# Kernel tuning notes

Hardware: AMD Instinct MI355X
Metric: run time of the kernel (lower is better)

Reference implementation:

```python
import jax, jax.numpy as jnp
import numpy as np

EMBED = 768
HEADS = 8


def setup_inputs() -> dict:
    key = jax.random.key(0)
    k1, k2, k3 = jax.random.split(key, 3)
    x = jax.random.normal(k1, (16, 1024, EMBED), dtype=jnp.float32)
    W_qkv = jax.random.normal(k2, (EMBED, 3 * EMBED), dtype=jnp.float32) * 0.02
    b_qkv = jnp.zeros((3 * EMBED,), dtype=jnp.float32)
    W_fc = jax.random.normal(k3, (EMBED, EMBED), dtype=jnp.float32) * 0.02
    b_fc = jnp.zeros((EMBED,), dtype=jnp.float32)
    return {"x": x, "W_qkv": W_qkv, "b_qkv": b_qkv, "W_fc": W_fc, "b_fc": b_fc}


def reference(x, W_qkv, b_qkv, W_fc, b_fc):
    b, n, e = x.shape
    h = HEADS
    d = e // h
    # fused QKV projection: (b, n, 3e) -> (b, n, h, d, 3) -> (3, b, h, n, d)
    qkv = x @ W_qkv + b_qkv
    qkv = qkv.reshape(b, n, h, d, 3)
    q, k, v = jnp.transpose(qkv, (4, 0, 2, 1, 3))
    # raw attention scores (b, h, n, n)
    qkt = jnp.einsum('bhid,bhjd->bhij', q, k)
    # NOTE: the original module computes softmax(QKT)/sqrt(E) into `attention`
    # but then uses the RAW scores QKT for the value contraction. We replicate
    # that faithfully; the softmax is dead code w.r.t. the output (p=0 dropout).
    attention = jax.nn.softmax(qkt, axis=-1) / jnp.sqrt(jnp.float32(e))  # unused, DCE'd
    z = jnp.einsum('bhik,bhkd->bhid', qkt, v)  # (b, h, n, d)
    z = jnp.transpose(z, (0, 2, 1, 3)).reshape(b, n, e)
    out = z @ W_fc + b_fc
    return out
```

## Files before the change

kernel.cpp:

```cpp
#include <hip/hip_runtime.h>

typedef unsigned short u16;
typedef __attribute__((ext_vector_type(8))) __bf16 bf16x8;
typedef __attribute__((ext_vector_type(4))) float f32x4;

__device__ __forceinline__ u16 f2bf(float f) {
  union { float f; unsigned u; } x; x.f = f;
  unsigned r = x.u + 0x7fffu + ((x.u >> 16) & 1u);
  return (u16)(r >> 16);
}

#define GLD16(g, l) __builtin_amdgcn_global_load_lds( \
    (__attribute__((address_space(1))) void*)(size_t)(g), \
    (__attribute__((address_space(3))) void*)(l), 16, 0, 0)

__global__ __launch_bounds__(256) void prep(const float* __restrict__ x,
                                            u16* __restrict__ xz,
                                            const float* __restrict__ Wqkv,
                                            u16* __restrict__ wqkvT,
                                            const float* __restrict__ Wfc,
                                            u16* __restrict__ wfcT) {
  __shared__ u16 tile[32][33];
  int bid = blockIdx.x;
  if (bid < 12288) {
    int i = bid * 256 + threadIdx.x;
    float4 v = ((const float4*)x)[i];
    ushort4 o;
    o.x = f2bf(v.x); o.y = f2bf(v.y); o.z = f2bf(v.z); o.w = f2bf(v.w);
    ((ushort4*)xz)[i] = o;
    return;
  }
  const float* in; u16* out; int C, perm, b2;
  if (bid < 14016) { b2 = bid - 12288; in = Wqkv; out = wqkvT; C = 2304; perm = 1; }
  else             { b2 = bid - 14016; in = Wfc;  out = wfcT;  C = 768;  perm = 0; }
  const int R = 768;
  int tilesC = C >> 5;
  int bc = b2 % tilesC, br = b2 / tilesC;
  int tx = threadIdx.x & 31, ty = threadIdx.x >> 5;
#pragma unroll
  for (int i = 0; i < 4; ++i)
    tile[ty + i * 8][tx] = f2bf(in[(size_t)(br * 32 + ty + i * 8) * C + bc * 32 + tx]);
  __syncthreads();
#pragma unroll
  for (int i = 0; i < 4; ++i) {
    int c = bc * 32 + ty + i * 8;
    int orow;
    if (perm) {
      int which = c % 3, h = c / 288, d = (c % 288) / 3;
      orow = which * 768 + h * 96 + d;
    } else {
      orow = c;
    }
    out[(size_t)orow * R + br * 32 + tx] = tile[tx][ty + i * 8];
  }
}

template <int EPI, int NF>
__global__ __launch_bounds__(512, 2) void gemm256(
    const u16* __restrict__ A, const u16* __restrict__ BT,
    const float* __restrict__ bias, int K, int lda, int ldb, int ldc,
    int tilesN, int cpx, size_t bstride, float* __restrict__ outf,
    u16* __restrict__ q_dst, u16* __restrict__ k_dst, u16* __restrict__ v_dst) {
  __shared__ u16 As[2][16384];
  __shared__ u16 Bs[2][NF * 4096];
  const int bid = blockIdx.x;
  const int swz = (bid & 7) * cpx + (bid >> 3);
  const int tr = swz / tilesN, tc = swz % tilesN;
  const int tid = threadIdx.x, lane = tid & 63, wv = tid >> 6;
  const int wr = wv >> 2, wc = wv & 3;
  const int l15 = lane & 15, lhi = lane >> 4;
  const int nt = K >> 6;
  const int region = tc / 3;

  BT += (size_t)((unsigned)(tr * 256) >> 10) * bstride;

  const u16 *srcA[4], *srcB[NF];
#pragma unroll
  for (int ch = 0; ch < 4; ++ch) {
    int g = ch * 512 + tid;
    int r = g >> 3;
    int c = (g & 7) ^ ((r >> 1) & 7);
    srcA[ch] = A + (size_t)(tr * 256 + r) * lda + c * 8;
  }
#pragma unroll
  for (int ch = 0; ch < NF; ++ch) {
    int g = ch * 512 + tid;
    int r = g >> 3;
    int c = (g & 7) ^ ((r >> 1) & 7);
    srcB[ch] = BT + (size_t)(tc * (64 * NF) + r) * ldb + c * 8;
  }
  int offa[8], offb[NF];
#pragma unroll
  for (int m = 0; m < 8; ++m) {
    int r = wr * 128 + m * 16 + l15;
    offa[m] = r * 64 + (lhi ^ ((r >> 1) & 7)) * 8;
  }
#pragma unroll
  for (int n = 0; n < NF; ++n) {
    int r = wc * (16 * NF) + n * 16 + l15;
    offb[n] = r * 64 + (lhi ^ ((r >> 1) & 7)) * 8;
  }

  float bv4[NF];
#pragma unroll
  for (int n = 0; n < NF; ++n) {
    int colg = tc * (64 * NF) + wc * (16 * NF) + n * 16 + l15;
    if constexpr (EPI == 0) {
      int lcol = colg - region * 768;
      bv4[n] = bias[(lcol / 96) * 288 + (lcol % 96) * 3 + region];
    } else {
      bv4[n] = bias[colg];
    }
  }

#define STAGE_A(t_) do { u16* Ad_ = (u16*)As[(t_) & 1]; int ko_ = (t_) * 64; \
    _Pragma("unroll") for (int ch = 0; ch < 4; ++ch) \
      GLD16(srcA[ch] + ko_, Ad_ + ((ch * 512 + wv * 64) * 8)); } while (0)
#define STAGE_B(t_) do { u16* Bd_ = (u16*)Bs[(t_) & 1]; int ko_ = (t_) * 64; \
    _Pragma("unroll") for (int ch = 0; ch < NF; ++ch) \
      GLD16(srcB[ch] + ko_, Bd_ + ((ch * 512 + wv * 64) * 8)); } while (0)

  bf16x8 af[4][2], bfv[NF][2];
#define RD_A(m_, slot_) do { \
    af[slot_][0] = *(const bf16x8*)&Ab[offa[m_]]; \
    af[slot_][1] = *(const bf16x8*)&Ab[offa[m_] ^ 32]; } while (0)
#define RD_B(n_) do { \
    bfv[n_][0] = *(const bf16x8*)&Bb[offb[n_]]; \
    bfv[n_][1] = *(const bf16x8*)&Bb[offb[n_] ^ 32]; } while (0)

  f32x4 acc[8][NF] = {};
#define CLUSTER(MB, NB, NN) do { \
    __builtin_amdgcn_s_setprio(1); \
    _Pragma("unroll") for (int mm = 0; mm < 4; ++mm) \
    _Pragma("unroll") for (int nn = 0; nn < (NN); ++nn) \
    _Pragma("unroll") for (int ks = 0; ks < 2; ++ks) \
      acc[(MB) + mm][(NB) + nn] = __builtin_amdgcn_mfma_f32_16x16x32_bf16( \
          af[mm][ks], bfv[(NB) + nn][ks], acc[(MB) + mm][(NB) + nn], 0, 0, 0); \
    __builtin_amdgcn_s_setprio(0); } while (0)
#define WAIT_LGKM_PIN() do { \
    asm volatile("s_waitcnt lgkmcnt(0)" ::: "memory"); \
    __builtin_amdgcn_sched_barrier(0); } while (0)

  STAGE_A(0); STAGE_B(0);
  asm volatile("s_waitcnt vmcnt(0)" ::: "memory");
  __builtin_amdgcn_s_barrier();

  for (int t = 0; t < nt; ++t) {
    const u16* Ab = As[t & 1];
    const u16* Bb = Bs[t & 1];
    RD_A(0, 0); RD_A(1, 1); RD_A(2, 2); RD_A(3, 3);
    RD_B(0); RD_B(1);
    if (t + 1 < nt) STAGE_A(t + 1);
    asm volatile("s_waitcnt lgkmcnt(8)" ::: "memory");
    __builtin_amdgcn_s_barrier();
    WAIT_LGKM_PIN();
    CLUSTER(0, 0, 2);
    __builtin_amdgcn_s_barrier();
#pragma unroll
    for (int n = 2; n < NF; ++n) RD_B(n);
    if (t + 1 < nt) STAGE_B(t + 1);
    __builtin_amdgcn_s_barrier();
    WAIT_LGKM_PIN();
    CLUSTER(0, 2, NF - 2);
    __builtin_amdgcn_s_barrier();
    RD_A(4, 0); RD_A(5, 1); RD_A(6, 2); RD_A(7, 3);
    __builtin_amdgcn_s_barrier();
    WAIT_LGKM_PIN();
    CLUSTER(4, 0, 2);
    __builtin_amdgcn_s_barrier();
    CLUSTER(4, 2, NF - 2);
    asm volatile("s_waitcnt vmcnt(0)" ::: "memory");
    __builtin_amdgcn_s_barrier();
  }
#undef STAGE_A
#undef STAGE_B
#undef RD_A
#undef RD_B
#undef CLUSTER
#undef WAIT_LGKM_PIN

  u16* dst16 = region == 0 ? q_dst : (region == 1 ? k_dst : v_dst);
#pragma unroll
  for (int m = 0; m < 8; ++m)
#pragma unroll
    for (int n = 0; n < NF; ++n) {
      int colg = tc * (64 * NF) + wc * (16 * NF) + n * 16 + l15;
      int lcol = colg - region * 768;
#pragma unroll
      for (int r = 0; r < 4; ++r) {
        int rowg = tr * 256 + wr * 128 + m * 16 + lhi * 4 + r;
        if constexpr (EPI == 0)
          dst16[(size_t)rowg * ldc + lcol] = f2bf(acc[m][n][r] + bv4[n]);
        else
          outf[(size_t)rowg * ldc + colg] = acc[m][n][r] + bv4[n];
      }
    }
}

__global__ __launch_bounds__(128) void kvm(const u16* __restrict__ kd,
                                           const u16* __restrict__ vd,
                                           u16* __restrict__ M) {
  __shared__ u16 kT[48][136];
  __shared__ u16 vT[96][136];
  const int bh = blockIdx.x >> 1, dh = blockIdx.x & 1;
  const int b = bh >> 3, h = bh & 7;
  const int tid = threadIdx.x, lane = tid & 63, nh = tid >> 6;
  const int l15 = lane & 15, lhi = lane >> 4;

  f32x4 acc[3][3] = {};

  for (int c = 0; c < 8; ++c) {
    const u16* kbase = kd + ((size_t)(b * 1024 + c * 128)) * 768 + h * 96 + dh * 48;
    const u16* vbase = vd + ((size_t)(b * 1024 + c * 128)) * 768 + h * 96;
    __syncthreads();
#pragma unroll
    for (int j = 0; j < 6; ++j) {
      int idx = j * 128 + tid;
      int n = idx / 6, gg = idx % 6;
      uint4 v = *(const uint4*)(kbase + (size_t)n * 768 + gg * 8);
      const u16* e = (const u16*)&v;
#pragma unroll
      for (int q = 0; q < 8; ++q) kT[gg * 8 + q][n] = e[q];
    }
#pragma unroll
    for (int j = 0; j < 12; ++j) {
      int idx = j * 128 + tid;
      int n = idx / 12, gg = idx % 12;
      uint4 v = *(const uint4*)(vbase + (size_t)n * 768 + gg * 8);
      const u16* e = (const u16*)&v;
#pragma unroll
      for (int q = 0; q < 8; ++q) vT[gg * 8 + q][n] = e[q];
    }
    __syncthreads();
#pragma unroll
    for (int ks = 0; ks < 4; ++ks) {
      bf16x8 a[3], bv[3];
#pragma unroll
      for (int mi = 0; mi < 3; ++mi)
        a[mi] = *(const bf16x8*)&kT[mi * 16 + l15][ks * 32 + lhi * 8];
#pragma unroll
      for (int nj = 0; nj < 3; ++nj)
        bv[nj] = *(const bf16x8*)&vT[nh * 48 + nj * 16 + l15][ks * 32 + lhi * 8];
#pragma unroll
      for (int mi = 0; mi < 3; ++mi)
#pragma unroll
        for (int nj = 0; nj < 3; ++nj)
          acc[mi][nj] = __builtin_amdgcn_mfma_f32_16x16x32_bf16(a[mi], bv[nj], acc[mi][nj], 0, 0, 0);
    }
  }

#pragma unroll
  for (int mi = 0; mi < 3; ++mi)
#pragma unroll
    for (int nj = 0; nj < 3; ++nj)
#pragma unroll
      for (int r = 0; r < 4; ++r)
        M[(size_t)bh * 9216 + (size_t)(dh * 48 + mi * 16 + lhi * 4 + r) * 96 +
          nh * 48 + nj * 16 + l15] = f2bf(acc[mi][nj][r]);
}

__global__ __launch_bounds__(512) void gkern(const u16* __restrict__ wfcT,
                                             const u16* __restrict__ M,
                                             u16* __restrict__ GT) {
  const int bh = blockIdx.x;
  const int b = bh >> 3, h = bh & 7;
  const int tid = threadIdx.x, lane = tid & 63, wv = tid >> 6;
  const int l15 = lane & 15, lhi = lane >> 4;
  const u16* Mb = M + (size_t)bh * 9216;
  f32x4 acc[6][6] = {};
#pragma unroll
  for (int ks = 0; ks < 3; ++ks) {
    bf16x8 a[6], bv[6];
#pragma unroll
    for (int fi = 0; fi < 6; ++fi)
      a[fi] = *(const bf16x8*)(wfcT + (size_t)(wv * 96 + fi * 16 + l15) * 768 +
                               h * 96 + ks * 32 + lhi * 8);
#pragma unroll
    for (int nj = 0; nj < 6; ++nj)
      bv[nj] = *(const bf16x8*)(Mb + (size_t)(nj * 16 + l15) * 96 + ks * 32 + lhi * 8);
#pragma unroll
    for (int fi = 0; fi < 6; ++fi)
#pragma unroll
      for (int nj = 0; nj < 6; ++nj)
        acc[fi][nj] = __builtin_amdgcn_mfma_f32_16x16x32_bf16(a[fi], bv[nj], acc[fi][nj], 0, 0, 0);
  }
#pragma unroll
  for (int fi = 0; fi < 6; ++fi)
#pragma unroll
    for (int nj = 0; nj < 6; ++nj)
#pragma unroll
      for (int r = 0; r < 4; ++r)
        GT[(size_t)b * 589824 + (size_t)(wv * 96 + fi * 16 + lhi * 4 + r) * 768 +
           h * 96 + nj * 16 + l15] = f2bf(acc[fi][nj][r]);
}

extern "C" void kernel_launch(void* const* d_in, const int* in_sizes, int n_in,
                              void* d_out, int out_size, void* d_ws, size_t ws_size,
                              hipStream_t stream) {
  const float* x    = (const float*)d_in[0];
  const float* Wqkv = (const float*)d_in[1];
  const float* bqkv = (const float*)d_in[2];
  const float* Wfc  = (const float*)d_in[3];
  const float* bfc  = (const float*)d_in[4];
  float* out = (float*)d_out;

  char* ws = (char*)d_ws;
  size_t off = 0;
  auto alloc = [&](size_t bytes) {
    void* p = ws + off;
    off += (bytes + 255) & ~(size_t)255;
    return p;
  };
  u16* xz    = (u16*)alloc(16384ull * 768 * 2);
  u16* wqkvT = (u16*)alloc(2304ull * 768 * 2);
  u16* wfcT  = (u16*)alloc(768ull * 768 * 2);
  u16* qb    = (u16*)alloc(16384ull * 768 * 2);
  u16* kb    = (u16*)alloc(16384ull * 768 * 2);
  u16* vb    = (u16*)alloc(16384ull * 768 * 2);

  prep<<<14592, 256, 0, stream>>>(x, xz, Wqkv, wqkvT, Wfc, wfcT);

  gemm256<0, 4><<<576, 512, 0, stream>>>(xz, wqkvT, bqkv, 768, 768, 768, 768,
                                         9, 72, 0, nullptr, qb, kb, vb);

  kvm<<<256, 128, 0, stream>>>(kb, vb, (u16*)wqkvT);

  gkern<<<128, 512, 0, stream>>>(wfcT, (u16*)wqkvT, vb);

  gemm256<1, 3><<<256, 512, 0, stream>>>(qb, vb, bfc, 768, 768, 768, 768,
                                         4, 32, 589824ull, out, nullptr, nullptr, nullptr);
}
```

Baseline: 166.1 us.

## Collapse GEMM main-loop barriers and prefetch all LDS fragments up front

Rewrites the GEMM inner loop so the only block-wide barrier is a single vmcnt(0) plus s_barrier at the top of each k-step. Both A and B global-to-LDS stages for the next tile are issued right after that barrier, instead of being interleaved between compute clusters. All A fragments (low and high halves) and all B fragments are read from LDS before the MFMA clusters run. Staged lgkmcnt waits let each MFMA cluster start as soon as its own operands arrive. This removes about seven barriers per iteration and gives the LDS reads more overlap with compute, at the cost of extra VGPRs for the second A-fragment register set.

```diff
diff --git a/kernel.cpp b/kernel.cpp
--- a/kernel.cpp
+++ b/kernel.cpp
@@ -120,64 +120,62 @@
     _Pragma("unroll") for (int ch = 0; ch < NF; ++ch) \
       GLD16(srcB[ch] + ko_, Bd_ + ((ch * 512 + wv * 64) * 8)); } while (0)
 
-  bf16x8 af[4][2], bfv[NF][2];
-#define RD_A(m_, slot_) do { \
-    af[slot_][0] = *(const bf16x8*)&Ab[offa[m_]]; \
-    af[slot_][1] = *(const bf16x8*)&Ab[offa[m_] ^ 32]; } while (0)
+  bf16x8 afl[4][2], afh[4][2], bfv[NF][2];
+#define RD_AL(m_) do { \
+    afl[m_][0] = *(const bf16x8*)&Ab[offa[m_]]; \
+    afl[m_][1] = *(const bf16x8*)&Ab[offa[m_] ^ 32]; } while (0)
+#define RD_AH(m_) do { \
+    afh[(m_) - 4][0] = *(const bf16x8*)&Ab[offa[m_]]; \
+    afh[(m_) - 4][1] = *(const bf16x8*)&Ab[offa[m_] ^ 32]; } while (0)
 #define RD_B(n_) do { \
     bfv[n_][0] = *(const bf16x8*)&Bb[offb[n_]]; \
     bfv[n_][1] = *(const bf16x8*)&Bb[offb[n_] ^ 32]; } while (0)
 
   f32x4 acc[8][NF] = {};
-#define CLUSTER(MB, NB, NN) do { \
+#define CLUSTER(AF, MB, NB, NN) do { \
     __builtin_amdgcn_s_setprio(1); \
     _Pragma("unroll") for (int mm = 0; mm < 4; ++mm) \
     _Pragma("unroll") for (int nn = 0; nn < (NN); ++nn) \
     _Pragma("unroll") for (int ks = 0; ks < 2; ++ks) \
       acc[(MB) + mm][(NB) + nn] = __builtin_amdgcn_mfma_f32_16x16x32_bf16( \
-          af[mm][ks], bfv[(NB) + nn][ks], acc[(MB) + mm][(NB) + nn], 0, 0, 0); \
+          AF[mm][ks], bfv[(NB) + nn][ks], acc[(MB) + mm][(NB) + nn], 0, 0, 0); \
     __builtin_amdgcn_s_setprio(0); } while (0)
-#define WAIT_LGKM_PIN() do { \
-    asm volatile("s_waitcnt lgkmcnt(0)" ::: "memory"); \
-    __builtin_amdgcn_sched_barrier(0); } while (0)
+#define SB0() __builtin_amdgcn_sched_barrier(0)
 
   STAGE_A(0); STAGE_B(0);
-  asm volatile("s_waitcnt vmcnt(0)" ::: "memory");
-  __builtin_amdgcn_s_barrier();
-
   for (int t = 0; t < nt; ++t) {
+    asm volatile("s_waitcnt vmcnt(0)" ::: "memory");
+    __builtin_amdgcn_s_barrier();
     const u16* Ab = As[t & 1];
     const u16* Bb = Bs[t & 1];
-    RD_A(0, 0); RD_A(1, 1); RD_A(2, 2); RD_A(3, 3);
+    if (t + 1 < nt) { STAGE_A(t + 1); STAGE_B(t + 1); }
+    RD_AL(0); RD_AL(1); RD_AL(2); RD_AL(3);
     RD_B(0); RD_B(1);
-    if (t + 1 < nt) STAGE_A(t + 1);
+    SB0();
+#pragma unroll
+    for (int n = 2; n < NF; ++n) RD_B(n);
+    SB0();
+    RD_AH(4); RD_AH(5); RD_AH(6); RD_AH(7);
+    SB0();
+    if constexpr (NF == 4) asm volatile("s_waitcnt lgkmcnt(12)" ::: "memory");
+    else                   asm volatile("s_waitcnt lgkmcnt(10)" ::: "memory");
+    SB0();
+    CLUSTER(afl, 0, 0, 2);
     asm volatile("s_waitcnt lgkmcnt(8)" ::: "memory");
-    __builtin_amdgcn_s_barrier();
-    WAIT_LGKM_PIN();
-    CLUSTER(0, 0, 2);
-    __builtin_amdgcn_s_barrier();
-#pragma unroll
-    for (int n = 2; n < NF; ++n) RD_B(n);
-    if (t + 1 < nt) STAGE_B(t + 1);
-    __builtin_amdgcn_s_barrier();
-    WAIT_LGKM_PIN();
-    CLUSTER(0, 2, NF - 2);
-    __builtin_amdgcn_s_barrier();
-    RD_A(4, 0); RD_A(5, 1); RD_A(6, 2); RD_A(7, 3);
-    __builtin_amdgcn_s_barrier();
-    WAIT_LGKM_PIN();
-    CLUSTER(4, 0, 2);
-    __builtin_amdgcn_s_barrier();
-    CLUSTER(4, 2, NF - 2);
-    asm volatile("s_waitcnt vmcnt(0)" ::: "memory");
-    __builtin_amdgcn_s_barrier();
+    SB0();
+    CLUSTER(afl, 0, 2, NF - 2);
+    asm volatile("s_waitcnt lgkmcnt(0)" ::: "memory");
+    SB0();
+    CLUSTER(afh, 4, 0, 2);
+    CLUSTER(afh, 4, 2, NF - 2);
   }
 #undef STAGE_A
 #undef STAGE_B
-#undef RD_A
+#undef RD_AL
+#undef RD_AH
 #undef RD_B
 #undef CLUSTER
-#undef WAIT_LGKM_PIN
+#undef SB0
 
   u16* dst16 = region == 0 ? q_dst : (region == 1 ? k_dst : v_dst);
 #pragma unroll
```

Measured after the change: 169.7 us. +2.2%, slower.
